# Optimization experiments

Hardware: AMD Instinct MI355X
Metric: run time of the kernel (lower is better)

The kernel has to match this reference:

```python
import jax, jax.numpy as jnp
import numpy as np

N = 50000      # nodes
E = 800000     # edges (before self-loops)
IN_C = 256
H1, H2 = 300, 100
OUT_C = 32


def _init_linear(key, fan_in, fan_out):
    kw, kb = jax.random.split(key)
    s = 1.0 / np.sqrt(fan_in)
    W = jax.random.uniform(kw, (fan_in, fan_out), minval=-s, maxval=s, dtype=jnp.float32)
    b = jax.random.uniform(kb, (fan_out,), minval=-s, maxval=s, dtype=jnp.float32)
    return W, b


def setup_inputs() -> dict:
    key = jax.random.key(0)
    ks = jax.random.split(key, 7)
    x = jax.random.normal(ks[0], (N, IN_C), dtype=jnp.float32)
    edge_index = jax.random.randint(ks[1], (2, E), 0, N, dtype=jnp.int64)
    W1, b1 = _init_linear(ks[2], IN_C, H1)
    W2, b2 = _init_linear(ks[3], H1, H2)
    W3, b3 = _init_linear(ks[4], H2, OUT_C)
    Wf1, bf1 = _init_linear(ks[5], OUT_C, 16)
    Wf2, bf2 = _init_linear(ks[6], 16, 1)
    return {"x": x, "edge_index": edge_index,
            "W1": W1, "b1": b1, "W2": W2, "b2": b2, "W3": W3, "b3": b3,
            "Wf1": Wf1, "bf1": bf1, "Wf2": Wf2, "bf2": bf2}


def _gcn_conv(x, W, b, row, col, norm, n):
    # PyG GCNConv: linear transform, then sym-normalized neighbor aggregation (+bias)
    h = x @ W                                   # [N, F_out]
    msg = h[col] * norm[:, None]                # gather + edge-wise scale, [E', F_out]
    agg = jax.ops.segment_sum(msg, row, num_segments=n)  # scatter-add back to nodes
    return agg + b


def reference(x, edge_index, W1, b1, W2, b2, W3, b3, Wf1, bf1, Wf2, bf2):
    n = x.shape[0]
    # add self-loops
    loop = jnp.arange(n, dtype=edge_index.dtype)
    row = jnp.concatenate([edge_index[0], loop])
    col = jnp.concatenate([edge_index[1], loop])
    # symmetric normalization D^{-1/2} (A+I) D^{-1/2}
    deg = jax.ops.segment_sum(jnp.ones_like(row, dtype=x.dtype), row, num_segments=n)
    dis = jnp.where(deg > 0, jax.lax.rsqrt(deg), 0.0)
    norm = dis[row] * dis[col]                  # [E']

    h = jax.nn.relu(_gcn_conv(x, W1, b1, row, col, norm, n))
    h = jax.nn.relu(_gcn_conv(h, W2, b2, row, col, norm, n))
    h = jax.nn.relu(_gcn_conv(h, W3, b3, row, col, norm, n))
    h = h @ Wf1 + bf1                           # [N, 16]
    return h @ Wf2 + bf2                        # [N, 1]
```

## Files before the change

### kernel.cpp

```cpp
#include <hip/hip_runtime.h>
#include <hip/hip_bf16.h>


#define WG 256

typedef __attribute__((ext_vector_type(4))) float f32x4;
typedef __attribute__((ext_vector_type(8))) short bf16x8;
typedef __attribute__((ext_vector_type(4))) unsigned short u16x4;

__device__ inline unsigned short f2bf(float v) {
    union { float f; unsigned u; } c; c.f = v;
    unsigned r = (c.u + 0x7fff + ((c.u >> 16) & 1)) >> 16;
    return (unsigned short)r;
}
__device__ inline float bf2f(unsigned short h) {
    union { unsigned u; float f; } c; c.u = ((unsigned)h) << 16;
    return c.f;
}


__global__ void count_kernel(const int* __restrict__ row, int* __restrict__ cnt, int E) {
    int e = blockIdx.x * blockDim.x + threadIdx.x;
    if (e < E) atomicAdd(&cnt[row[e]], 1);
}

__global__ void dis_kernel(const int* __restrict__ cnt, float* __restrict__ dis, int n) {
    int i = blockIdx.x * blockDim.x + threadIdx.x;
    if (i < n) {
        float d = (float)(cnt[i] + 1);
        dis[i] = 1.0f / sqrtf(d);
    }
}

__global__ __launch_bounds__(1024) void scan_kernel(const int* __restrict__ cnt,
                                                    int* __restrict__ rowstart, int n) {
    __shared__ int wsum[16];
    __shared__ int carry;
    const int tid = threadIdx.x;
    const int lane = tid & 63, wv = tid >> 6;
    if (tid == 0) { rowstart[0] = 0; carry = 0; }
    __syncthreads();
    for (int base = 0; base < n; base += 1024) {
        int i = base + tid;
        int v = (i < n) ? (cnt[i] + 1) : 0;
        int s = v;
        #pragma unroll
        for (int off = 1; off < 64; off <<= 1) {
            int t = __shfl_up(s, off);
            if (lane >= off) s += t;
        }
        if (lane == 63) wsum[wv] = s;
        __syncthreads();
        if (wv == 0 && lane < 16) {
            int ws = wsum[lane];
            int t = ws;
            #pragma unroll
            for (int off = 1; off < 16; off <<= 1) {
                int u = __shfl_up(t, off);
                if (lane >= off) t += u;
            }
            wsum[lane] = t - ws;
        }
        __syncthreads();
        int tp = carry;
        if (i < n) rowstart[i + 1] = tp + wsum[wv] + s;
        __syncthreads();
        if (tid == 1023) carry = tp + wsum[15] + s;
        __syncthreads();
    }
}

__global__ void selfloop_kernel(const int* __restrict__ rowstart, const float* __restrict__ dis,
                                int* __restrict__ edge_dst, float* __restrict__ edge_norm,
                                int* __restrict__ fill, int n) {
    int i = blockIdx.x * blockDim.x + threadIdx.x;
    if (i < n) {
        int p = rowstart[i];
        edge_dst[p] = i;
        float d = dis[i];
        edge_norm[p] = d * d;
        fill[i] = 1;
    }
}

__global__ void scatter_kernel(const int* __restrict__ row, const int* __restrict__ col,
                               const int* __restrict__ rowstart, const float* __restrict__ dis,
                               int* __restrict__ edge_dst, float* __restrict__ edge_norm,
                               int* __restrict__ fill, int E) {
    int e = blockIdx.x * blockDim.x + threadIdx.x;
    if (e < E) {
        int r = row[e], c = col[e];
        int pos = rowstart[r] + atomicAdd(&fill[r], 1);
        edge_dst[pos] = c;
        edge_norm[pos] = dis[r] * dis[c];
    }
}


__global__ void convB_kernel(const float* __restrict__ W,
                             unsigned short* __restrict__ bth, unsigned short* __restrict__ btl,
                             int K, int N, int Kpad, int Npad) {
    int idx = blockIdx.x * blockDim.x + threadIdx.x;
    int total = (Kpad / 8) * Npad * 8;
    if (idx >= total) return;
    int i = idx & 7;
    int rest = idx >> 3;
    int n = rest % Npad;
    int qg = rest / Npad;
    int k = qg * 8 + i;
    float v = (k < K && n < N) ? W[k * N + n] : 0.f;
    unsigned short h = f2bf(v);
    unsigned short l = f2bf(v - bf2f(h));
    bth[idx] = h;
    btl[idx] = l;
}


__global__ __launch_bounds__(256) void mfma_gemm(const float* __restrict__ A,
                                                 const unsigned short* __restrict__ Bth,
                                                 const unsigned short* __restrict__ Btl,
                                                 float* __restrict__ C,
                                                 const float* __restrict__ bias,
                                                 int M, int Kpad, int Npad, int Nbias, int dorelu) {
    __shared__ unsigned short Ah[4 * 128 * 8];
    __shared__ unsigned short Al[4 * 128 * 8];
    const int tid  = threadIdx.x;
    const int lane = tid & 63;
    const int wid  = tid >> 6;
    const int wm   = (wid >> 1) * 64;
    const int wn   = (wid & 1) * 32;
    const int m0   = blockIdx.y * 128;
    const int n0   = blockIdx.x * 64;
    const int q    = lane >> 4;
    const int lr   = lane & 15;

    f32x4 acc[4][2];
    #pragma unroll
    for (int i = 0; i < 4; ++i)
        #pragma unroll
        for (int j = 0; j < 2; ++j) {
            f32x4 z = {0.f, 0.f, 0.f, 0.f};
            acc[i][j] = z;
        }

    f32x4 rg[4];

    auto load_tile = [&](int k0) {
        #pragma unroll
        for (int it = 0; it < 4; ++it) {
            int lin = it * 256 + tid;
            int r   = lin >> 3;
            int f4  = lin & 7;
            int row = m0 + r;
            int k   = k0 + f4 * 4;
            f32x4 v = {0.f, 0.f, 0.f, 0.f};
            if (row < M) v = *(const f32x4*)(A + (size_t)row * Kpad + k);
            rg[it] = v;
        }
    };

    auto write_stage = [&]() {
        #pragma unroll
        for (int it = 0; it < 4; ++it) {
            int lin  = it * 256 + tid;
            int r    = lin >> 3;
            int f4   = lin & 7;
            int qq   = f4 >> 1;
            int half = f4 & 1;
            u16x4 hi, lo;
            #pragma unroll
            for (int e = 0; e < 4; ++e) {
                float v = rg[it][e];
                unsigned short h = f2bf(v);
                hi[e] = h;
                lo[e] = f2bf(v - bf2f(h));
            }
            int off = (qq * 128 + r) * 8 + half * 4;
            *(u16x4*)(Ah + off) = hi;
            *(u16x4*)(Al + off) = lo;
        }
    };

    load_tile(0);
    const int nk = Kpad >> 5;
    for (int t = 0; t < nk; ++t) {
        if (t) __syncthreads();
        write_stage();
        __syncthreads();
        if (t + 1 < nk) load_tile((t + 1) * 32);

        bf16x8 ah[4], al[4];
        #pragma unroll
        for (int mf = 0; mf < 4; ++mf) {
            int off = (q * 128 + wm + mf * 16 + lr) * 8;
            ah[mf] = *(const bf16x8*)(Ah + off);
            al[mf] = *(const bf16x8*)(Al + off);
        }
        bf16x8 bh[2], bl[2];
        int qg = t * 4 + q;
        #pragma unroll
        for (int nf = 0; nf < 2; ++nf) {
            int n = n0 + wn + nf * 16 + lr;
            size_t coff = ((size_t)qg * Npad + n) * 8;
            bh[nf] = *(const bf16x8*)(Bth + coff);
            bl[nf] = *(const bf16x8*)(Btl + coff);
        }
        #pragma unroll
        for (int mf = 0; mf < 4; ++mf)
            #pragma unroll
            for (int nf = 0; nf < 2; ++nf)
                acc[mf][nf] = __builtin_amdgcn_mfma_f32_16x16x32_bf16(ah[mf], bh[nf], acc[mf][nf], 0, 0, 0);
        #pragma unroll
        for (int mf = 0; mf < 4; ++mf)
            #pragma unroll
            for (int nf = 0; nf < 2; ++nf)
                acc[mf][nf] = __builtin_amdgcn_mfma_f32_16x16x32_bf16(ah[mf], bl[nf], acc[mf][nf], 0, 0, 0);
        #pragma unroll
        for (int mf = 0; mf < 4; ++mf)
            #pragma unroll
            for (int nf = 0; nf < 2; ++nf)
                acc[mf][nf] = __builtin_amdgcn_mfma_f32_16x16x32_bf16(al[mf], bh[nf], acc[mf][nf], 0, 0, 0);
    }

    #pragma unroll
    for (int nf = 0; nf < 2; ++nf) {
        int col = n0 + wn + nf * 16 + lr;
        float bb = (bias != nullptr && col < Nbias) ? bias[col] : 0.f;
        #pragma unroll
        for (int mf = 0; mf < 4; ++mf) {
            int row_base = m0 + wm + mf * 16 + (lane >> 4) * 4;
            #pragma unroll
            for (int r = 0; r < 4; ++r) {
                int row = row_base + r;
                if (row < M) {
                    float v = acc[mf][nf][r] + bb;
                    if (dorelu) v = fmaxf(v, 0.f);
                    C[(size_t)row * Npad + col] = v;
                }
            }
        }
    }
}


template <int R4, int EPW>
__global__ __launch_bounds__(256) void agg_kernel(const float* __restrict__ src,
                                                  const int* __restrict__ rowstart,
                                                  const int* __restrict__ edge_dst,
                                                  const float* __restrict__ edge_norm,
                                                  const float* __restrict__ bias,
                                                  float* __restrict__ out,
                                                  int out_stride, int fout, int dorelu,
                                                  int nnodes) {
    const int wid  = threadIdx.x >> 6;
    const int node = blockIdx.x * 4 + wid;
    if (node >= nnodes) return;
    const int lane = threadIdx.x & 63;
    const int g    = lane / R4;
    const int lg   = lane % R4;
    const int start = rowstart[node], end = rowstart[node + 1];
    const f32x4* s4 = (const f32x4*)src;
    f32x4 acc = {0.f, 0.f, 0.f, 0.f};

    for (int base = start; base < end; base += 64) {
        int nb = end - base;
        if (nb > 64) nb = 64;
        int ge = base + lane;
        int idx = (lane < nb) ? edge_dst[ge] : 0;
        float w = (lane < nb) ? edge_norm[ge] : 0.f;
        int iters = (nb + EPW - 1) / EPW;
        int j = 0;
        for (; j + 4 <= iters; j += 4) {
            int c0 = __shfl(idx, (j + 0) * EPW + g); float w0 = __shfl(w, (j + 0) * EPW + g);
            int c1 = __shfl(idx, (j + 1) * EPW + g); float w1 = __shfl(w, (j + 1) * EPW + g);
            int c2 = __shfl(idx, (j + 2) * EPW + g); float w2 = __shfl(w, (j + 2) * EPW + g);
            int c3 = __shfl(idx, (j + 3) * EPW + g); float w3 = __shfl(w, (j + 3) * EPW + g);
            f32x4 v0 = s4[(size_t)c0 * R4 + lg];
            f32x4 v1 = s4[(size_t)c1 * R4 + lg];
            f32x4 v2 = s4[(size_t)c2 * R4 + lg];
            f32x4 v3 = s4[(size_t)c3 * R4 + lg];
            acc += v0 * w0;
            acc += v1 * w1;
            acc += v2 * w2;
            acc += v3 * w3;
        }
        for (; j < iters; ++j) {
            int sl = j * EPW + g;
            int c = __shfl(idx, sl); float w0 = __shfl(w, sl);
            f32x4 v = s4[(size_t)c * R4 + lg];
            acc += v * w0;
        }
    }

    #pragma unroll
    for (int d = R4; d < 64; d <<= 1) {
        #pragma unroll
        for (int k = 0; k < 4; ++k) acc[k] += __shfl_xor(acc[k], d);
    }

    if (g == 0) {
        int f0 = lg * 4;
        if (f0 < out_stride) {
            f32x4 v = acc;
            if (bias != nullptr) {
                #pragma unroll
                for (int e = 0; e < 4; ++e) {
                    int f = f0 + e;
                    if (f < fout) {
                        float t = v[e] + bias[f];
                        if (dorelu) t = fmaxf(t, 0.f);
                        v[e] = t;
                    }
                }
            }
            *(f32x4*)(out + (size_t)node * out_stride + f0) = v;
        }
    }
}


__global__ void final_kernel(const float* __restrict__ a3,
                             const float* __restrict__ Wf1, const float* __restrict__ bf1,
                             const float* __restrict__ Wf2, const float* __restrict__ bf2,
                             float* __restrict__ out, int n, int C, int H) {
    int i = blockIdx.x * blockDim.x + threadIdx.x;
    if (i >= n) return;
    const float* xr = a3 + (size_t)i * C;
    float hbuf[16];
    for (int j = 0; j < H; ++j) hbuf[j] = bf1[j];
    for (int k = 0; k < C; ++k) {
        float xv = xr[k];
        for (int j = 0; j < H; ++j) hbuf[j] += xv * Wf1[k * H + j];
    }
    float o = bf2[0];
    for (int j = 0; j < H; ++j) o += hbuf[j] * Wf2[j];
    out[i] = o;
}


extern "C" void kernel_launch(void* const* d_in, const int* in_sizes, int n_in,
                              void* d_out, int out_size, void* d_ws, size_t ws_size,
                              hipStream_t stream) {
    const float* x   = (const float*)d_in[0];
    const int*   ei  = (const int*)d_in[1];
    const float* W1  = (const float*)d_in[2];
    const float* b1  = (const float*)d_in[3];
    const float* W2  = (const float*)d_in[4];
    const float* b2  = (const float*)d_in[5];
    const float* W3  = (const float*)d_in[6];
    const float* b3  = (const float*)d_in[7];
    const float* Wf1 = (const float*)d_in[8];
    const float* bf1 = (const float*)d_in[9];
    const float* Wf2 = (const float*)d_in[10];
    const float* bf2 = (const float*)d_in[11];
    float* out = (float*)d_out;

    const int N    = out_size;
    const int E    = in_sizes[1] / 2;
    const int IN_C = in_sizes[0] / N;
    const int H1   = in_sizes[3];
    const int H2   = in_sizes[5];
    const int OUTC = in_sizes[7];
    const int F1   = in_sizes[9];
    const int EL   = E + N;

    const int KP1 = 256, NP1 = 320;
    const int KP2 = 320, NP2 = 128;
    const int KP3 = 128, NP3 = 64;

    const int* row = ei;
    const int* col = ei + E;

    size_t off = 0;
    auto alloc = [&](size_t bytes) {
        size_t o = off;
        off += (bytes + 255) & ~(size_t)255;
        return o;
    };
    char* ws = (char*)d_ws;
    int*   cnt      = (int*)  (ws + alloc((size_t)N * 4));
    int*   fill     = (int*)  (ws + alloc((size_t)N * 4));
    float* dis      = (float*)(ws + alloc((size_t)N * 4));
    int*   rowstart = (int*)  (ws + alloc((size_t)(N + 1) * 4));
    int*   edge_dst = (int*)  (ws + alloc((size_t)EL * 4));
    float* edge_nrm = (float*)(ws + alloc((size_t)EL * 4));
    unsigned short* Bt1h = (unsigned short*)(ws + alloc((size_t)(KP1/8) * NP1 * 8 * 2));
    unsigned short* Bt1l = (unsigned short*)(ws + alloc((size_t)(KP1/8) * NP1 * 8 * 2));
    unsigned short* Bt2h = (unsigned short*)(ws + alloc((size_t)(KP2/8) * NP2 * 8 * 2));
    unsigned short* Bt2l = (unsigned short*)(ws + alloc((size_t)(KP2/8) * NP2 * 8 * 2));
    unsigned short* Bt3h = (unsigned short*)(ws + alloc((size_t)(KP3/8) * NP3 * 8 * 2));
    unsigned short* Bt3l = (unsigned short*)(ws + alloc((size_t)(KP3/8) * NP3 * 8 * 2));
    float* bufA = (float*)(ws + alloc((size_t)N * KP1 * 4));
    float* bufB = (float*)(ws + alloc((size_t)N * NP1 * 4));

    float* agg_x = bufA;
    float* a1    = bufB;
    float* h2    = bufA;
    float* a2    = bufA + (size_t)N * NP2;
    float* h3    = bufB;
    float* a3    = bufB + (size_t)N * NP3;

    const int gN = (N + WG - 1) / WG;
    const int gE = (E + WG - 1) / WG;
    const int gAgg = (N + 3) / 4;

    hipMemsetAsync(cnt, 0, (size_t)N * 4, stream);
    count_kernel<<<gE, WG, 0, stream>>>(row, cnt, E);
    dis_kernel<<<gN, WG, 0, stream>>>(cnt, dis, N);
    scan_kernel<<<1, 1024, 0, stream>>>(cnt, rowstart, N);
    selfloop_kernel<<<gN, WG, 0, stream>>>(rowstart, dis, edge_dst, edge_nrm, fill, N);
    scatter_kernel<<<gE, WG, 0, stream>>>(row, col, rowstart, dis, edge_dst, edge_nrm, fill, E);

    {
        int t1 = (KP1/8) * NP1 * 8;
        convB_kernel<<<(t1 + WG - 1) / WG, WG, 0, stream>>>(W1, Bt1h, Bt1l, IN_C, H1, KP1, NP1);
        int t2 = (KP2/8) * NP2 * 8;
        convB_kernel<<<(t2 + WG - 1) / WG, WG, 0, stream>>>(W2, Bt2h, Bt2l, H1, H2, KP2, NP2);
        int t3 = (KP3/8) * NP3 * 8;
        convB_kernel<<<(t3 + WG - 1) / WG, WG, 0, stream>>>(W3, Bt3h, Bt3l, H2, OUTC, KP3, NP3);
    }

    const int MB = (N + 127) / 128;

    agg_kernel<64, 1><<<gAgg, WG, 0, stream>>>(x, rowstart, edge_dst, edge_nrm,
                                               nullptr, agg_x, KP1, KP1, 0, N);
    mfma_gemm<<<dim3(NP1 / 64, MB), 256, 0, stream>>>(agg_x, Bt1h, Bt1l, a1, b1,
                                                      N, KP1, NP1, H1, 1);
    mfma_gemm<<<dim3(NP2 / 64, MB), 256, 0, stream>>>(a1, Bt2h, Bt2l, h2, nullptr,
                                                      N, KP2, NP2, 0, 0);
    agg_kernel<32, 2><<<gAgg, WG, 0, stream>>>(h2, rowstart, edge_dst, edge_nrm,
                                               b2, a2, NP2, H2, 1, N);
    mfma_gemm<<<dim3(NP3 / 64, MB), 256, 0, stream>>>(a2, Bt3h, Bt3l, h3, nullptr,
                                                      N, KP3, NP3, 0, 0);
    agg_kernel<16, 4><<<gAgg, WG, 0, stream>>>(h3, rowstart, edge_dst, edge_nrm,
                                               b3, a3, OUTC, OUTC, 1, N);
    final_kernel<<<gN, WG, 0, stream>>>(a3, Wf1, bf1, Wf2, bf2, out, N, OUTC, F1);
}
```

Measured before the change: 591.7 us.

## Pre-split GEMM A operands into bf16 hi/lo in producer epilogues

Producer kernels (aggregation and GEMM epilogues) now write their outputs directly as separate bf16 hi and lo planes, so the GEMM loads 16-bit data and copies it straight into shared memory instead of reading fp32 and splitting per tile. The hi/lo split switches from round-to-nearest to truncation, and the shared-memory tile gets a row swizzle to reduce bank conflicts. This removes conversion ALU work from the GEMM inner loop and avoids re-splitting the A tile once per column block. Global traffic stays about the same, since two 16-bit planes are the size of one fp32 array. Truncating the hi part loses a little precision in the split, and the buffer aliasing in the workspace is rearranged.

```diff
diff --git a/kernel.cpp b/kernel.cpp
--- a/kernel.cpp
+++ b/kernel.cpp
@@ -7,6 +7,7 @@
 typedef __attribute__((ext_vector_type(4))) float f32x4;
 typedef __attribute__((ext_vector_type(8))) short bf16x8;
 typedef __attribute__((ext_vector_type(4))) unsigned short u16x4;
+typedef __attribute__((ext_vector_type(8))) unsigned short u16x8;
 
 __device__ inline unsigned short f2bf(float v) {
     union { float f; unsigned u; } c; c.f = v;
@@ -16,6 +17,12 @@
 __device__ inline float bf2f(unsigned short h) {
     union { unsigned u; float f; } c; c.u = ((unsigned)h) << 16;
     return c.f;
+}
+__device__ inline void splitbf(float v, unsigned short& h, unsigned short& l) {
+    unsigned u = __float_as_uint(v);
+    h = (unsigned short)(u >> 16);
+    float hf = __uint_as_float(u & 0xffff0000u);
+    l = (unsigned short)(__float_as_uint(v - hf) >> 16);
 }
 
 
@@ -116,12 +123,15 @@
 }
 
 
-__global__ __launch_bounds__(256) void mfma_gemm(const float* __restrict__ A,
-                                                 const unsigned short* __restrict__ Bth,
-                                                 const unsigned short* __restrict__ Btl,
-                                                 float* __restrict__ C,
-                                                 const float* __restrict__ bias,
-                                                 int M, int Kpad, int Npad, int Nbias, int dorelu) {
+__global__ __launch_bounds__(256) void mfma_gemm_sp(const unsigned short* __restrict__ Ahg,
+                                                    const unsigned short* __restrict__ Alg,
+                                                    const unsigned short* __restrict__ Bth,
+                                                    const unsigned short* __restrict__ Btl,
+                                                    float* __restrict__ Cf,
+                                                    unsigned short* __restrict__ Ch,
+                                                    unsigned short* __restrict__ Cl,
+                                                    const float* __restrict__ bias,
+                                                    int M, int Kpad, int Npad, int Nbias, int dorelu) {
     __shared__ unsigned short Ah[4 * 128 * 8];
     __shared__ unsigned short Al[4 * 128 * 8];
     const int tid  = threadIdx.x;
@@ -143,18 +153,18 @@
             acc[i][j] = z;
         }
 
-    f32x4 rg[4];
+    u16x8 rg[4];
 
     auto load_tile = [&](int k0) {
         #pragma unroll
         for (int it = 0; it < 4; ++it) {
-            int lin = it * 256 + tid;
-            int r   = lin >> 3;
-            int f4  = lin & 7;
+            int lin = (it & 1) * 256 + tid;
+            int r   = lin >> 2;
+            int qq  = lin & 3;
+            const unsigned short* src = (it < 2) ? Ahg : Alg;
             int row = m0 + r;
-            int k   = k0 + f4 * 4;
-            f32x4 v = {0.f, 0.f, 0.f, 0.f};
-            if (row < M) v = *(const f32x4*)(A + (size_t)row * Kpad + k);
+            u16x8 v = {0, 0, 0, 0, 0, 0, 0, 0};
+            if (row < M) v = *(const u16x8*)(src + (size_t)row * Kpad + k0 + qq * 8);
             rg[it] = v;
         }
     };
@@ -162,22 +172,12 @@
     auto write_stage = [&]() {
         #pragma unroll
         for (int it = 0; it < 4; ++it) {
-            int lin  = it * 256 + tid;
-            int r    = lin >> 3;
-            int f4   = lin & 7;
-            int qq   = f4 >> 1;
-            int half = f4 & 1;
-            u16x4 hi, lo;
-            #pragma unroll
-            for (int e = 0; e < 4; ++e) {
-                float v = rg[it][e];
-                unsigned short h = f2bf(v);
-                hi[e] = h;
-                lo[e] = f2bf(v - bf2f(h));
-            }
-            int off = (qq * 128 + r) * 8 + half * 4;
-            *(u16x4*)(Ah + off) = hi;
-            *(u16x4*)(Al + off) = lo;
+            int lin = (it & 1) * 256 + tid;
+            int r   = lin >> 2;
+            int qq  = lin & 3;
+            unsigned short* dst = (it < 2) ? Ah : Al;
+            int rs = (r + 2 * qq) & 127;
+            *(u16x8*)(dst + (qq * 128 + rs) * 8) = rg[it];
         }
     };
 
@@ -192,7 +192,9 @@
         bf16x8 ah[4], al[4];
         #pragma unroll
         for (int mf = 0; mf < 4; ++mf) {
-            int off = (q * 128 + wm + mf * 16 + lr) * 8;
+            int row = wm + mf * 16 + lr;
+            int rs  = (row + 2 * q) & 127;
+            int off = (q * 128 + rs) * 8;
             ah[mf] = *(const bf16x8*)(Ah + off);
             al[mf] = *(const bf16x8*)(Al + off);
         }
@@ -232,10 +234,17 @@
             #pragma unroll
             for (int r = 0; r < 4; ++r) {
                 int row = row_base + r;
-                if (row < M) {
-                    float v = acc[mf][nf][r] + bb;
-                    if (dorelu) v = fmaxf(v, 0.f);
-                    C[(size_t)row * Npad + col] = v;
+                if (row >= M) continue;
+                float v = acc[mf][nf][r] + bb;
+                if (dorelu) v = fmaxf(v, 0.f);
+                size_t o = (size_t)row * Npad + col;
+                if (Cf != nullptr) {
+                    Cf[o] = v;
+                } else {
+                    unsigned short h, l;
+                    splitbf(v, h, l);
+                    Ch[o] = h;
+                    Cl[o] = l;
                 }
             }
         }
@@ -249,7 +258,9 @@
                                                   const int* __restrict__ edge_dst,
                                                   const float* __restrict__ edge_norm,
                                                   const float* __restrict__ bias,
-                                                  float* __restrict__ out,
+                                                  float* __restrict__ outf,
+                                                  unsigned short* __restrict__ outh,
+                                                  unsigned short* __restrict__ outl,
                                                   int out_stride, int fout, int dorelu,
                                                   int nnodes) {
     const int wid  = threadIdx.x >> 6;
@@ -313,7 +324,21 @@
                     }
                 }
             }
-            *(f32x4*)(out + (size_t)node * out_stride + f0) = v;
+            size_t o = (size_t)node * out_stride + f0;
+            if (outh != nullptr) {
+                u16x4 hv, lv;
+                #pragma unroll
+                for (int e = 0; e < 4; ++e) {
+                    unsigned short hh, ll;
+                    splitbf(v[e], hh, ll);
+                    hv[e] = hh;
+                    lv[e] = ll;
+                }
+                *(u16x4*)(outh + o) = hv;
+                *(u16x4*)(outl + o) = lv;
+            } else {
+                *(f32x4*)(outf + o) = v;
+            }
         }
     }
 }
@@ -390,15 +415,18 @@
     unsigned short* Bt2l = (unsigned short*)(ws + alloc((size_t)(KP2/8) * NP2 * 8 * 2));
     unsigned short* Bt3h = (unsigned short*)(ws + alloc((size_t)(KP3/8) * NP3 * 8 * 2));
     unsigned short* Bt3l = (unsigned short*)(ws + alloc((size_t)(KP3/8) * NP3 * 8 * 2));
-    float* bufA = (float*)(ws + alloc((size_t)N * KP1 * 4));
-    float* bufB = (float*)(ws + alloc((size_t)N * NP1 * 4));
-
-    float* agg_x = bufA;
-    float* a1    = bufB;
-    float* h2    = bufA;
-    float* a2    = bufA + (size_t)N * NP2;
-    float* h3    = bufB;
-    float* a3    = bufB + (size_t)N * NP3;
+    char* bufP = ws + alloc((size_t)N * KP1 * 4);
+    char* bufQ = ws + alloc((size_t)N * KP2 * 4);
+
+    unsigned short* agg_xh = (unsigned short*)bufP;
+    unsigned short* agg_xl = (unsigned short*)(bufP + (size_t)N * KP1 * 2);
+    unsigned short* a1h    = (unsigned short*)bufQ;
+    unsigned short* a1l    = (unsigned short*)(bufQ + (size_t)N * KP2 * 2);
+    float*          h2     = (float*)bufP;
+    unsigned short* a2h    = (unsigned short*)(bufP + (size_t)N * NP2 * 4);
+    unsigned short* a2l    = (unsigned short*)(bufP + (size_t)N * NP2 * 4 + (size_t)N * KP3 * 2);
+    float*          h3     = (float*)bufP;
+    float*          a3     = (float*)(bufP + (size_t)N * NP3 * 4);
 
     const int gN = (N + WG - 1) / WG;
     const int gE = (E + WG - 1) / WG;
@@ -423,16 +451,22 @@
     const int MB = (N + 127) / 128;
 
     agg_kernel<64, 1><<<gAgg, WG, 0, stream>>>(x, rowstart, edge_dst, edge_nrm,
-                                               nullptr, agg_x, KP1, KP1, 0, N);
-    mfma_gemm<<<dim3(NP1 / 64, MB), 256, 0, stream>>>(agg_x, Bt1h, Bt1l, a1, b1,
-                                                      N, KP1, NP1, H1, 1);
-    mfma_gemm<<<dim3(NP2 / 64, MB), 256, 0, stream>>>(a1, Bt2h, Bt2l, h2, nullptr,
-                                                      N, KP2, NP2, 0, 0);
+                                               nullptr, nullptr, agg_xh, agg_xl,
+                                               KP1, KP1, 0, N);
+    mfma_gemm_sp<<<dim3(NP1 / 64, MB), 256, 0, stream>>>(agg_xh, agg_xl, Bt1h, Bt1l,
+                                                         nullptr, a1h, a1l, b1,
+                                                         N, KP1, NP1, H1, 1);
+    mfma_gemm_sp<<<dim3(NP2 / 64, MB), 256, 0, stream>>>(a1h, a1l, Bt2h, Bt2l,
+                                                         h2, nullptr, nullptr, nullptr,
+                                                         N, KP2, NP2, 0, 0);
     agg_kernel<32, 2><<<gAgg, WG, 0, stream>>>(h2, rowstart, edge_dst, edge_nrm,
-                                               b2, a2, NP2, H2, 1, N);
-    mfma_gemm<<<dim3(NP3 / 64, MB), 256, 0, stream>>>(a2, Bt3h, Bt3l, h3, nullptr,
-                                                      N, KP3, NP3, 0, 0);
+                                               b2, nullptr, a2h, a2l,
+                                               KP3, H2, 1, N);
+    mfma_gemm_sp<<<dim3(NP3 / 64, MB), 256, 0, stream>>>(a2h, a2l, Bt3h, Bt3l,
+                                                         h3, nullptr, nullptr, nullptr,
+                                                         N, KP3, NP3, 0, 0);
     agg_kernel<16, 4><<<gAgg, WG, 0, stream>>>(h3, rowstart, edge_dst, edge_nrm,
-                                               b3, a3, OUTC, OUTC, 1, N);
+                                               b3, a3, nullptr, nullptr,
+                                               OUTC, OUTC, 1, N);
     final_kernel<<<gN, WG, 0, stream>>>(a3, Wf1, bf1, Wf2, bf2, out, N, OUTC, F1);
 }
```

New measurement: 599.6 us. Within noise of the previous version (+1.3%).
